# Kernel optimization log

Measured on AMD Instinct MI355X. Metric: run time of the kernel, lower is better.

## Reference

```python
import jax, jax.numpy as jnp
import numpy as np

EMBED_DIM = 1024
NUM_HEADS = 16
HEAD_DIM = EMBED_DIM // NUM_HEADS
MAX_LEN = 1000  # default in RelativePositionalEncoding
B, T = 4, 1024


def setup_inputs() -> dict:
    key = jax.random.key(0)
    ks = jax.random.split(key, 12)
    s = 0.02
    d = EMBED_DIM
    return {
        "query": jax.random.normal(ks[0], (B, T, d), jnp.float32),
        "key": jax.random.normal(ks[1], (B, T, d), jnp.float32),
        "value": jax.random.normal(ks[2], (B, T, d), jnp.float32),
        "Wq": jax.random.normal(ks[3], (d, d), jnp.float32) * s,
        "bq": jnp.zeros((d,), jnp.float32),
        "Wk": jax.random.normal(ks[4], (d, d), jnp.float32) * s,
        "bk": jnp.zeros((d,), jnp.float32),
        "Wv": jax.random.normal(ks[5], (d, d), jnp.float32) * s,
        "bv": jnp.zeros((d,), jnp.float32),
        "Wo": jax.random.normal(ks[6], (d, d), jnp.float32) * s,
        "bo": jnp.zeros((d,), jnp.float32),
        "rel_emb": jax.random.normal(ks[7], (2 * MAX_LEN - 1, HEAD_DIM), jnp.float32) * s,
    }


def reference(query, key, value, Wq, bq, Wk, bk, Wv, bv, Wo, bo, rel_emb):
    Bq, Tq, C = query.shape
    H, hd = NUM_HEADS, HEAD_DIM
    # projections -> [B, H, T, hd]
    q = (query @ Wq.T + bq).reshape(Bq, Tq, H, hd).transpose(0, 2, 1, 3)
    k = (key @ Wk.T + bk).reshape(Bq, Tq, H, hd).transpose(0, 2, 1, 3)
    v = (value @ Wv.T + bv).reshape(Bq, Tq, H, hd).transpose(0, 2, 1, 3)
    # content scores [B, H, T, T]
    attn_scores = jnp.einsum('bhtd,bhsd->bhts', q, k)
    # relative positional embedding gather: E[t, s] = rel_emb[clamp(s - t + max_len - 1)]
    pos = jnp.arange(Tq)
    idx = jnp.clip(pos[None, :] - pos[:, None] + MAX_LEN - 1, 0, 2 * MAX_LEN - 2)
    E = rel_emb[idx]  # [T, T, hd]
    # NOTE: original uses raw (unprojected) query reshaped into heads for rel-pos scores
    rpe_q = query.transpose(1, 0, 2).reshape(Tq, Bq * H, hd)  # [T, B*H, hd]
    rpe = jnp.einsum('tnd,tsd->nts', rpe_q, E).reshape(Bq, H, Tq, Tq)
    # faithful to original: divide by scale = hd**-0.5 (i.e. multiply by sqrt(hd))
    scale = hd ** (-0.5)
    attn = (attn_scores + rpe) / scale
    attn_weights = jax.nn.softmax(attn, axis=-1)
    out = jnp.einsum('bhts,bhsd->bhtd', attn_weights, v)
    out = out.transpose(0, 2, 1, 3).reshape(Bq, Tq, C)
    return out @ Wo.T + bo
```

## Files before the change

kernel.cpp:

```cpp
#include <hip/hip_runtime.h>
#include <math.h>

typedef _Float16 h16;
typedef __attribute__((ext_vector_type(4))) _Float16 half4;
typedef __attribute__((ext_vector_type(8))) _Float16 half8;
typedef __attribute__((ext_vector_type(4))) float f32x4;

#define AS1 __attribute__((address_space(1)))
#define AS3 __attribute__((address_space(3)))
#define MFMA16(a, b, c) __builtin_amdgcn_mfma_f32_16x16x32_f16((a), (b), (c), 0, 0, 0)

__device__ __forceinline__ float ex2(float x) {
  return __builtin_amdgcn_exp2f(x);
}

__global__ __launch_bounds__(256) void convert(
    const float* __restrict__ q, const float* __restrict__ k,
    const float* __restrict__ v, const float* __restrict__ Wq,
    const float* __restrict__ Wk, const float* __restrict__ Wv,
    const float* __restrict__ Wo, const float* __restrict__ rel, h16* q16c,
    h16* k16c, h16* v16c, h16* Wq16, h16* Wk16, h16* Wv16, h16* Wo16,
    h16* relb) {
  const int i = blockIdx.x * 256 + threadIdx.x;
  if (i >= 4226304) return;
  const float* src;
  h16* dst;
  int off;
  if (i < 1048576) {
    src = q; dst = q16c; off = i;
  } else if (i < 2097152) {
    src = k; dst = k16c; off = i - 1048576;
  } else if (i < 3145728) {
    src = v; dst = v16c; off = i - 2097152;
  } else if (i < 3407872) {
    src = Wq; dst = Wq16; off = i - 3145728;
  } else if (i < 3670016) {
    src = Wk; dst = Wk16; off = i - 3407872;
  } else if (i < 3932160) {
    src = Wv; dst = Wv16; off = i - 3670016;
  } else if (i < 4194304) {
    src = Wo; dst = Wo16; off = i - 3932160;
  } else {
    off = i - 4194304;
    half4 hv = (half4){(h16)0.f, (h16)0.f, (h16)0.f, (h16)0.f};
    if (off < 31984) {
      float4 f = *(const float4*)(rel + (size_t)off * 4);
      hv = (half4){(h16)f.x, (h16)f.y, (h16)f.z, (h16)f.w};
    }
    *(half4*)(relb + (size_t)off * 4) = hv;
    return;
  }
  float4 f = *(const float4*)(src + (size_t)off * 4);
  *(half4*)(dst + (size_t)off * 4) =
      (half4){(h16)f.x, (h16)f.y, (h16)f.z, (h16)f.w};
}

template <int MODE>
__device__ __forceinline__ void gemm128_body(const h16* __restrict__ A,
                                             const h16* __restrict__ Bt,
                                             const float* __restrict__ bias,
                                             h16* __restrict__ outp) {
  __shared__ alignas(16) h16 As[128 * 32];
  __shared__ alignas(16) h16 Bs[128 * 32];
  const int tid = threadIdx.x;
  const int wave = tid >> 6;
  const int lane = tid & 63;
  const int wm = wave >> 1, wn = wave & 1;
  const int tm0 = blockIdx.x * 128, tn0 = blockIdx.y * 128;
  const int lrow = lane & 15;
  const int kq = lane >> 4;
  const int srow = lane >> 2;
  const int scol = (lane & 3) * 8;

  f32x4 acc[4][4];
#pragma unroll
  for (int i = 0; i < 4; ++i)
#pragma unroll
    for (int j = 0; j < 4; ++j) acc[i][j] = (f32x4){0.f, 0.f, 0.f, 0.f};

  for (int k0 = 0; k0 < 1024; k0 += 32) {
    __syncthreads();
#pragma unroll
    for (int rep = 0; rep < 2; ++rep) {
      const int cw = wave * 2 + rep;
      const int row = cw * 16 + srow;
      __builtin_amdgcn_global_load_lds(
          (const AS1 void*)(A + (size_t)(tm0 + row) * 1024 + k0 + scol),
          (AS3 void*)(As + cw * 512), 16, 0, 0);
      __builtin_amdgcn_global_load_lds(
          (const AS1 void*)(Bt + (size_t)(tn0 + row) * 1024 + k0 + scol),
          (AS3 void*)(Bs + cw * 512), 16, 0, 0);
    }
    __syncthreads();
    half8 af[4], bf[4];
#pragma unroll
    for (int i = 0; i < 4; ++i)
      af[i] = *(const half8*)(As + (wm * 64 + i * 16 + lrow) * 32 + kq * 8);
#pragma unroll
    for (int j = 0; j < 4; ++j)
      bf[j] = *(const half8*)(Bs + (wn * 64 + j * 16 + lrow) * 32 + kq * 8);
#pragma unroll
    for (int i = 0; i < 4; ++i)
#pragma unroll
      for (int j = 0; j < 4; ++j) acc[i][j] = MFMA16(af[i], bf[j], acc[i][j]);
  }

#pragma unroll
  for (int j = 0; j < 4; ++j) {
    const int n = tn0 + wn * 64 + j * 16 + lrow;
    const float bval = bias[n];
#pragma unroll
    for (int i = 0; i < 4; ++i) {
      const int rowb = wm * 64 + i * 16 + kq * 4;
#pragma unroll
      for (int r = 0; r < 4; ++r) {
        const int m = tm0 + rowb + r;
        const float val = acc[i][j][r] + bval;
        const int b = m >> 10, t = m & 1023, hh = n >> 6, d = n & 63;
        if (MODE == 0) {
          outp[((size_t)((b << 4) + hh) << 16) + (t << 6) + d] = (h16)val;
        } else {
          outp[(((size_t)((b << 4) + hh) * 64 + d) << 10) + t] = (h16)val;
        }
      }
    }
  }
}

__global__ __launch_bounds__(256) void qkv_gemm(
    const h16* q16c, const h16* k16c, const h16* v16c, const h16* Wq16,
    const h16* Wk16, const h16* Wv16, const float* bq, const float* bk,
    const float* bv, h16* q16, h16* k16, h16* vt16) {
  const int z = blockIdx.z;
  const h16* A = (z == 0) ? q16c : (z == 1) ? k16c : v16c;
  const h16* Bt = (z == 0) ? Wq16 : (z == 1) ? Wk16 : Wv16;
  const float* bias = (z == 0) ? bq : (z == 1) ? bk : bv;
  if (z == 2)
    gemm128_body<1>(A, Bt, bias, vt16);
  else
    gemm128_body<0>(A, Bt, bias, (z == 0) ? q16 : k16);
}

__global__ __launch_bounds__(256) void out_gemm(const h16* __restrict__ A,
                                                const h16* __restrict__ Bt,
                                                const float* __restrict__ bo,
                                                float* __restrict__ out) {
  __shared__ alignas(16) h16 As[64 * 32];
  __shared__ alignas(16) h16 Bs[128 * 32];
  const int tid = threadIdx.x;
  const int wave = tid >> 6;
  const int lane = tid & 63;
  const int wm = wave >> 1, wn = wave & 1;
  const int tm0 = blockIdx.x * 64, tn0 = blockIdx.y * 128;
  const int lrow = lane & 15;
  const int kq = lane >> 4;
  const int srow = lane >> 2;
  const int scol = (lane & 3) * 8;

  f32x4 acc[2][4];
#pragma unroll
  for (int i = 0; i < 2; ++i)
#pragma unroll
    for (int j = 0; j < 4; ++j) acc[i][j] = (f32x4){0.f, 0.f, 0.f, 0.f};

  for (int k0 = 0; k0 < 1024; k0 += 32) {
    __syncthreads();
    {
      const int row = wave * 16 + srow;
      __builtin_amdgcn_global_load_lds(
          (const AS1 void*)(A + (size_t)(tm0 + row) * 1024 + k0 + scol),
          (AS3 void*)(As + wave * 512), 16, 0, 0);
    }
#pragma unroll
    for (int rep = 0; rep < 2; ++rep) {
      const int cw = wave * 2 + rep;
      const int row = cw * 16 + srow;
      __builtin_amdgcn_global_load_lds(
          (const AS1 void*)(Bt + (size_t)(tn0 + row) * 1024 + k0 + scol),
          (AS3 void*)(Bs + cw * 512), 16, 0, 0);
    }
    __syncthreads();
    half8 af[2], bf[4];
#pragma unroll
    for (int i = 0; i < 2; ++i)
      af[i] = *(const half8*)(As + (wm * 32 + i * 16 + lrow) * 32 + kq * 8);
#pragma unroll
    for (int j = 0; j < 4; ++j)
      bf[j] = *(const half8*)(Bs + (wn * 64 + j * 16 + lrow) * 32 + kq * 8);
#pragma unroll
    for (int i = 0; i < 2; ++i)
#pragma unroll
      for (int j = 0; j < 4; ++j) acc[i][j] = MFMA16(af[i], bf[j], acc[i][j]);
  }

#pragma unroll
  for (int j = 0; j < 4; ++j) {
    const int n = tn0 + wn * 64 + j * 16 + lrow;
    const float bval = bo[n];
#pragma unroll
    for (int i = 0; i < 2; ++i) {
      const int rowb = wm * 32 + i * 16 + kq * 4;
#pragma unroll
      for (int r = 0; r < 4; ++r) {
        const int m = tm0 + rowb + r;
        out[(size_t)m * 1024 + n] = acc[i][j][r] + bval;
      }
    }
  }
}

__global__ __launch_bounds__(256, 4) void attn_mfma(
    const h16* __restrict__ q16, const h16* __restrict__ k16,
    const h16* __restrict__ vt16, const h16* __restrict__ q16c,
    const h16* __restrict__ relb, h16* __restrict__ ao) {
  __shared__ alignas(16) h16 Kh[4096];
  __shared__ alignas(16) h16 Rl[8192];
  __shared__ alignas(16) h16 VtS[4096];
  __shared__ alignas(16) h16 Ps[4096];

  const int bid = blockIdx.x;
  const int ttile = bid & 15;
  const int bh = bid >> 4;
  const int b = bh >> 4, h = bh & 15;
  const int t0 = ttile << 6;
  const int tid = threadIdx.x;
  const int w = tid >> 6;
  const int lane = tid & 63;
  const int l15 = lane & 15;
  const int kq = lane >> 4;

  const int tq = t0 + w * 16 + l15;
  half8 aq[2], arq[2];
#pragma unroll
  for (int ks = 0; ks < 2; ++ks) {
    aq[ks] =
        *(const half8*)(q16 + ((size_t)bh * 1024 + tq) * 64 + kq * 8 + ks * 32);
    arq[ks] = *(const half8*)(q16c + ((size_t)(b * 1024 + tq)) * 1024 + h * 64 +
                              kq * 8 + ks * 32);
  }

  float m2[4], ls[4];
  f32x4 O[4];
#pragma unroll
  for (int r = 0; r < 4; ++r) {
    m2[r] = -1e30f;
    ls[r] = 0.f;
  }
#pragma unroll
  for (int db = 0; db < 4; ++db) O[db] = (f32x4){0.f, 0.f, 0.f, 0.f};

  const int trow = w * 16 + kq * 4;

  for (int s0 = 0; s0 < 1024; s0 += 64) {
    __syncthreads();
    for (int i = tid; i < 512; i += 256) {
      const int row = i >> 3, c = i & 7;
      *(half8*)(Kh + row * 64 + ((c ^ (row & 7)) << 3)) = *(const half8*)(
          k16 + ((size_t)(bh * 1024 + s0 + row)) * 64 + c * 8);
    }
    for (int i = tid; i < 512; i += 256) {
      const int row = i >> 3, c = i & 7;
      *(half8*)(VtS + row * 64 + ((c ^ (row & 7)) << 3)) = *(const half8*)(
          vt16 + ((size_t)bh * 64 + row) * 1024 + s0 + c * 8);
    }
    const int base = s0 - t0 + 999 - 63;
    for (int i = tid; i < 1024; i += 256) {
      const int row = i >> 3, c = i & 7;
      int ridx = base + row;
      ridx = ridx < 0 ? 0 : (ridx > 1998 ? 1998 : ridx);
      *(half8*)(Rl + row * 64 + ((c ^ (row & 7)) << 3)) =
          *(const half8*)(relb + (size_t)ridx * 64 + c * 8);
    }
    __syncthreads();

    f32x4 S[4];
#pragma unroll
    for (int ns = 0; ns < 4; ++ns) {
      f32x4 s = (f32x4){0.f, 0.f, 0.f, 0.f};
      const int kr = ns * 16 + l15;
#pragma unroll
      for (int ks = 0; ks < 2; ++ks) {
        const int c = ((ks * 4 + kq) ^ (kr & 7)) << 3;
        s = MFMA16(aq[ks], *(const half8*)(Kh + kr * 64 + c), s);
      }
      S[ns] = s;
    }

    f32x4 G[5];
#pragma unroll
    for (int gi = 0; gi < 5; ++gi) {
      f32x4 g = (f32x4){0.f, 0.f, 0.f, 0.f};
      const int ur = (3 - w + gi) * 16 + l15;
#pragma unroll
      for (int ks = 0; ks < 2; ++ks) {
        const int c = ((ks * 4 + kq) ^ (ur & 7)) << 3;
        g = MFMA16(arq[ks], *(const half8*)(Rl + ur * 64 + c), g);
      }
      G[gi] = g;
    }

    const float SC = 11.54156032711170727f;
    const int C0 = 63 - w * 16 - kq * 4;
#pragma unroll
    for (int ns = 0; ns < 4; ++ns) {
#pragma unroll
      for (int r = 0; r < 4; ++r) {
        const int u = l15 + C0 + ns * 16 - r;
        const int src = (kq << 4) | (u & 15);
        const int gsel = (u >> 4) + w - 3;
        const float v0 = __shfl(G[ns][r], src, 64);
        const float v1 = __shfl(G[(ns + 1) <= 4 ? (ns + 1) : 4][r], src, 64);
        const float g = (gsel == ns) ? v0 : v1;
        S[ns][r] = (S[ns][r] + g) * SC;
      }
    }

#pragma unroll
    for (int r = 0; r < 4; ++r) {
      float mx = fmaxf(fmaxf(S[0][r], S[1][r]), fmaxf(S[2][r], S[3][r]));
      mx = fmaxf(mx, __shfl_xor(mx, 1));
      mx = fmaxf(mx, __shfl_xor(mx, 2));
      mx = fmaxf(mx, __shfl_xor(mx, 4));
      mx = fmaxf(mx, __shfl_xor(mx, 8));
      const float nm = fmaxf(m2[r], mx);
      const float al = ex2(m2[r] - nm);
      m2[r] = nm;
      const int t = trow + r;
      float rs = 0.f;
#pragma unroll
      for (int ns = 0; ns < 4; ++ns) {
        const float p = ex2(S[ns][r] - nm);
        rs += p;
        const int sl = ns * 16 + l15;
        Ps[t * 64 + (((sl >> 3) ^ (t & 7)) << 3) + (sl & 7)] = (h16)p;
      }
      rs += __shfl_xor(rs, 1);
      rs += __shfl_xor(rs, 2);
      rs += __shfl_xor(rs, 4);
      rs += __shfl_xor(rs, 8);
      ls[r] = ls[r] * al + rs;
      O[0][r] *= al;
      O[1][r] *= al;
      O[2][r] *= al;
      O[3][r] *= al;
    }

    const int tp = w * 16 + l15;
#pragma unroll
    for (int ks = 0; ks < 2; ++ks) {
      const int ca = ((ks * 4 + kq) ^ (tp & 7)) << 3;
      half8 pa = *(const half8*)(Ps + tp * 64 + ca);
#pragma unroll
      for (int db = 0; db < 4; ++db) {
        const int vr = db * 16 + l15;
        const int cb = ((ks * 4 + kq) ^ (vr & 7)) << 3;
        O[db] = MFMA16(pa, *(const half8*)(VtS + vr * 64 + cb), O[db]);
      }
    }
  }

#pragma unroll
  for (int r = 0; r < 4; ++r) {
    const float inv = 1.f / ls[r];
    const int t = t0 + trow + r;
    h16* op = ao + ((size_t)(b * 1024 + t)) * 1024 + h * 64;
#pragma unroll
    for (int db = 0; db < 4; ++db) op[db * 16 + l15] = (h16)(O[db][r] * inv);
  }
}

extern "C" void kernel_launch(void* const* d_in, const int* in_sizes, int n_in,
                              void* d_out, int out_size, void* d_ws,
                              size_t ws_size, hipStream_t stream) {
  const float* query = (const float*)d_in[0];
  const float* key = (const float*)d_in[1];
  const float* value = (const float*)d_in[2];
  const float* Wq = (const float*)d_in[3];
  const float* bq = (const float*)d_in[4];
  const float* Wk = (const float*)d_in[5];
  const float* bk = (const float*)d_in[6];
  const float* Wv = (const float*)d_in[7];
  const float* bv = (const float*)d_in[8];
  const float* Wo = (const float*)d_in[9];
  const float* bo = (const float*)d_in[10];
  const float* rel = (const float*)d_in[11];

  char* ws = (char*)d_ws;
  h16* q16c = (h16*)ws;
  h16* k16c = (h16*)(ws + ((size_t)8 << 20));
  h16* v16c = (h16*)(ws + ((size_t)16 << 20));
  h16* Wq16 = (h16*)(ws + ((size_t)24 << 20));
  h16* Wk16 = (h16*)(ws + ((size_t)26 << 20));
  h16* Wv16 = (h16*)(ws + ((size_t)28 << 20));
  h16* Wo16 = (h16*)(ws + ((size_t)30 << 20));
  h16* q16 = (h16*)(ws + ((size_t)32 << 20));
  h16* k16 = (h16*)(ws + ((size_t)40 << 20));
  h16* vt16 = (h16*)(ws + ((size_t)48 << 20));
  h16* relb = (h16*)(ws + ((size_t)56 << 20));
  h16* ao = k16c;
  float* out = (float*)d_out;

  convert<<<16509, 256, 0, stream>>>(query, key, value, Wq, Wk, Wv, Wo, rel,
                                     q16c, k16c, v16c, Wq16, Wk16, Wv16, Wo16,
                                     relb);
  qkv_gemm<<<dim3(32, 8, 3), 256, 0, stream>>>(q16c, k16c, v16c, Wq16, Wk16,
                                               Wv16, bq, bk, bv, q16, k16,
                                               vt16);
  attn_mfma<<<1024, 256, 0, stream>>>(q16, k16, vt16, q16c, relb, ao);
  out_gemm<<<dim3(64, 8), 256, 0, stream>>>(ao, Wo16, bo, out);
}
```

Before: 289.3 us.

## Use direct global-to-LDS loads, DPP reductions, bpermute shift, and MFMA priority

The K, V^T and relative-embedding tile loads now use global_load_lds, which writes straight into shared memory instead of going through registers, with the XOR swizzle applied on the source address. The row max and sum reductions use DPP lane swizzles in place of shfl_xor. The relative-position shift is rebuilt as one ds_bpermute per element with the source tile chosen beforehand, replacing two shuffles and a select. s_setprio raises wave priority around the MFMA blocks. Together these aim to cut register traffic and cross-lane shuffle overhead in the attention inner loop, at the cost of depending on exact DPP and LDS-DMA semantics for correctness.

Result: faster. 257.6 us (-11.0%).

```diff
diff --git a/kernel.cpp b/kernel.cpp
--- a/kernel.cpp
+++ b/kernel.cpp
@@ -12,6 +12,26 @@
 
 __device__ __forceinline__ float ex2(float x) {
   return __builtin_amdgcn_exp2f(x);
+}
+
+template <int CTRL>
+__device__ __forceinline__ float dppf(float x) {
+  return __int_as_float(__builtin_amdgcn_update_dpp(
+      0, __float_as_int(x), CTRL, 0xF, 0xF, true));
+}
+__device__ __forceinline__ float rmax16(float x) {
+  x = fmaxf(x, dppf<0xB1>(x));
+  x = fmaxf(x, dppf<0x4E>(x));
+  x = fmaxf(x, dppf<0x124>(x));
+  x = fmaxf(x, dppf<0x128>(x));
+  return x;
+}
+__device__ __forceinline__ float rsum16(float x) {
+  x += dppf<0xB1>(x);
+  x += dppf<0x4E>(x);
+  x += dppf<0x124>(x);
+  x += dppf<0x128>(x);
+  return x;
 }
 
 __global__ __launch_bounds__(256) void convert(
@@ -253,26 +273,42 @@
 
   for (int s0 = 0; s0 < 1024; s0 += 64) {
     __syncthreads();
-    for (int i = tid; i < 512; i += 256) {
-      const int row = i >> 3, c = i & 7;
-      *(half8*)(Kh + row * 64 + ((c ^ (row & 7)) << 3)) = *(const half8*)(
-          k16 + ((size_t)(bh * 1024 + s0 + row)) * 64 + c * 8);
-    }
-    for (int i = tid; i < 512; i += 256) {
-      const int row = i >> 3, c = i & 7;
-      *(half8*)(VtS + row * 64 + ((c ^ (row & 7)) << 3)) = *(const half8*)(
-          vt16 + ((size_t)bh * 64 + row) * 1024 + s0 + c * 8);
+
+#pragma unroll
+    for (int p = 0; p < 2; ++p) {
+      const int a = (w * 2 + p) * 64 + lane;
+      const int row = a >> 3;
+      const int c = (a & 7) ^ (row & 7);
+      __builtin_amdgcn_global_load_lds(
+          (const AS1 void*)(k16 + ((size_t)(bh * 1024 + s0 + row)) * 64 +
+                            c * 8),
+          (AS3 void*)(Kh + (w * 2 + p) * 512), 16, 0, 0);
+    }
+#pragma unroll
+    for (int p = 0; p < 2; ++p) {
+      const int a = (w * 2 + p) * 64 + lane;
+      const int row = a >> 3;
+      const int c = (a & 7) ^ (row & 7);
+      __builtin_amdgcn_global_load_lds(
+          (const AS1 void*)(vt16 + ((size_t)(bh * 64 + row)) * 1024 + s0 +
+                            c * 8),
+          (AS3 void*)(VtS + (w * 2 + p) * 512), 16, 0, 0);
     }
     const int base = s0 - t0 + 999 - 63;
-    for (int i = tid; i < 1024; i += 256) {
-      const int row = i >> 3, c = i & 7;
+#pragma unroll
+    for (int p = 0; p < 4; ++p) {
+      const int a = (w * 4 + p) * 64 + lane;
+      const int row = a >> 3;
+      const int c = (a & 7) ^ (row & 7);
       int ridx = base + row;
       ridx = ridx < 0 ? 0 : (ridx > 1998 ? 1998 : ridx);
-      *(half8*)(Rl + row * 64 + ((c ^ (row & 7)) << 3)) =
-          *(const half8*)(relb + (size_t)ridx * 64 + c * 8);
-    }
-    __syncthreads();
-
+      __builtin_amdgcn_global_load_lds(
+          (const AS1 void*)(relb + (size_t)ridx * 64 + c * 8),
+          (AS3 void*)(Rl + (w * 4 + p) * 512), 16, 0, 0);
+    }
+    __syncthreads();
+
+    __builtin_amdgcn_s_setprio(1);
     f32x4 S[4];
 #pragma unroll
     for (int ns = 0; ns < 4; ++ns) {
@@ -298,19 +334,19 @@
       }
       G[gi] = g;
     }
+    __builtin_amdgcn_s_setprio(0);
 
     const float SC = 11.54156032711170727f;
-    const int C0 = 63 - w * 16 - kq * 4;
-#pragma unroll
-    for (int ns = 0; ns < 4; ++ns) {
-#pragma unroll
-      for (int r = 0; r < 4; ++r) {
-        const int u = l15 + C0 + ns * 16 - r;
-        const int src = (kq << 4) | (u & 15);
-        const int gsel = (u >> 4) + w - 3;
-        const float v0 = __shfl(G[ns][r], src, 64);
-        const float v1 = __shfl(G[(ns + 1) <= 4 ? (ns + 1) : 4][r], src, 64);
-        const float g = (gsel == ns) ? v0 : v1;
+#pragma unroll
+    for (int r = 0; r < 4; ++r) {
+      const int Cm = 15 - kq * 4 - r;
+      const int sladdr = ((kq << 4) | ((l15 + Cm) & 15)) << 2;
+      const bool nolap = (l15 >= Cm);
+#pragma unroll
+      for (int ns = 0; ns < 4; ++ns) {
+        const float mv = nolap ? G[ns][r] : G[ns + 1][r];
+        const float g = __int_as_float(
+            __builtin_amdgcn_ds_bpermute(sladdr, __float_as_int(mv)));
         S[ns][r] = (S[ns][r] + g) * SC;
       }
     }
@@ -318,10 +354,7 @@
 #pragma unroll
     for (int r = 0; r < 4; ++r) {
       float mx = fmaxf(fmaxf(S[0][r], S[1][r]), fmaxf(S[2][r], S[3][r]));
-      mx = fmaxf(mx, __shfl_xor(mx, 1));
-      mx = fmaxf(mx, __shfl_xor(mx, 2));
-      mx = fmaxf(mx, __shfl_xor(mx, 4));
-      mx = fmaxf(mx, __shfl_xor(mx, 8));
+      mx = rmax16(mx);
       const float nm = fmaxf(m2[r], mx);
       const float al = ex2(m2[r] - nm);
       m2[r] = nm;
@@ -334,10 +367,7 @@
         const int sl = ns * 16 + l15;
         Ps[t * 64 + (((sl >> 3) ^ (t & 7)) << 3) + (sl & 7)] = (h16)p;
       }
-      rs += __shfl_xor(rs, 1);
-      rs += __shfl_xor(rs, 2);
-      rs += __shfl_xor(rs, 4);
-      rs += __shfl_xor(rs, 8);
+      rs = rsum16(rs);
       ls[r] = ls[r] * al + rs;
       O[0][r] *= al;
       O[1][r] *= al;
@@ -346,6 +376,7 @@
     }
 
     const int tp = w * 16 + l15;
+    __builtin_amdgcn_s_setprio(1);
 #pragma unroll
     for (int ks = 0; ks < 2; ++ks) {
       const int ca = ((ks * 4 + kq) ^ (tp & 7)) << 3;
@@ -357,6 +388,7 @@
         O[db] = MFMA16(pa, *(const half8*)(VtS + vr * 64 + cb), O[db]);
       }
     }
+    __builtin_amdgcn_s_setprio(0);
   }
 
 #pragma unroll
```
